# Performance work log

Hardware: AMD Instinct MI355X
Metric: run time of the kernel (lower is better)

Reference implementation:

```python
import jax, jax.numpy as jnp
import numpy as np

B, L, C = 128, 512, 8   # batch, stream length, path channels
DEPTH = 4
N_OUT = 10
SIG_DIM = C + C**2 + C**3 + C**4  # signatory.signature_channels(C, 4) = 4680


def setup_inputs() -> dict:
    key = jax.random.key(0)
    kx, kw, kb = jax.random.split(key, 3)
    X = jax.random.normal(kx, (B, L, C), dtype=jnp.float32) * 0.1
    W = jax.random.normal(kw, (N_OUT, SIG_DIM), dtype=jnp.float32) / np.sqrt(SIG_DIM)
    b = jax.random.normal(kb, (N_OUT,), dtype=jnp.float32) * 0.01
    return {"X": X, "W": W, "b": b}


def _signature_depth4(X):
    """Depth-4 path signature (Chen's relation scan), matching signatory.signature.

    X: (B, L, C) -> (B, C + C^2 + C^3 + C^4) with levels concatenated in order.
    """
    dx = X[:, 1:, :] - X[:, :-1, :]          # (B, L-1, C) path increments
    dx = jnp.swapaxes(dx, 0, 1)              # (L-1, B, C) for scan over stream
    bsz, c = X.shape[0], X.shape[2]

    def step(carry, v):
        s1, s2, s3, s4 = carry
        # exp(v) in the tensor algebra: e_k = v^{\otimes k} / k!
        e1 = v
        e2 = jnp.einsum('bi,bj->bij', v, v) / 2.0
        e3 = jnp.einsum('bij,bk->bijk', e2, v) / 3.0
        e4 = jnp.einsum('bijk,bl->bijkl', e3, v) / 4.0
        # Chen's relation: (S \otimes exp(v))_k = sum_i S_i \otimes e_{k-i}
        n1 = s1 + e1
        n2 = s2 + jnp.einsum('bi,bj->bij', s1, e1) + e2
        n3 = (s3 + jnp.einsum('bij,bk->bijk', s2, e1)
              + jnp.einsum('bi,bjk->bijk', s1, e2) + e3)
        n4 = (s4 + jnp.einsum('bijk,bl->bijkl', s3, e1)
              + jnp.einsum('bij,bkl->bijkl', s2, e2)
              + jnp.einsum('bi,bjkl->bijkl', s1, e3) + e4)
        return (n1, n2, n3, n4), None

    init = (jnp.zeros((bsz, c), X.dtype),
            jnp.zeros((bsz, c, c), X.dtype),
            jnp.zeros((bsz, c, c, c), X.dtype),
            jnp.zeros((bsz, c, c, c, c), X.dtype))
    (s1, s2, s3, s4), _ = jax.lax.scan(step, init, dx)
    return jnp.concatenate([s1.reshape(bsz, -1), s2.reshape(bsz, -1),
                            s3.reshape(bsz, -1), s4.reshape(bsz, -1)], axis=-1)


def reference(X, W, b):
    sig = _signature_depth4(X)               # (B, SIG_DIM)
    out = sig @ W.T + b                      # nn.Linear
    return out.reshape(-1, N_OUT)
```

## Files before the change

### kernel.cpp

```cpp
#include <hip/hip_runtime.h>

#define BATCH 128
#define LEN 512
#define N_OUT 10
#define SIG_DIM 4680
#define OFF2W 8
#define OFF3W 72
#define OFF4W 584
#define B2OFF 8
#define B3OFF 72
#define B4OFF 648
#define BUFSZ 4808

typedef float v4f __attribute__((ext_vector_type(4)));

__device__ __forceinline__ void stage_fat(float* __restrict__ buf,
                                          float s1, float s2,
                                          const float s3[8], const float s4[8][8],
                                          int lane) {
    if ((lane & 7) == 0) buf[lane >> 3] = s1;
    buf[B2OFF + lane] = s2;
    #pragma unroll
    for (int k = 0; k < 8; ++k) buf[B3OFF + lane * 9 + k] = s3[k];
    #pragma unroll
    for (int k = 0; k < 8; ++k) {
        #pragma unroll
        for (int l = 0; l < 8; ++l)
            buf[B4OFF + lane * 65 + k * 8 + l] = s4[k][l];
    }
}

__device__ __forceinline__ void combine_fat(float& A1, float& A2,
                                            float A3[8], float A4[8][8],
                                            const float* __restrict__ buf,
                                            int i, int j, int lane) {
    float B1[8];
    #pragma unroll
    for (int l = 0; l < 8; ++l) B1[l] = buf[l];
    #pragma unroll
    for (int k = 0; k < 8; ++k) {
        #pragma unroll
        for (int l = 0; l < 8; ++l) {
            A4[k][l] += A3[k] * B1[l]
                      + A2 * buf[B2OFF + k * 8 + l]
                      + A1 * buf[B3OFF + (j * 8 + k) * 9 + l]
                      + buf[B4OFF + lane * 65 + k * 8 + l];
        }
    }
    #pragma unroll
    for (int k = 0; k < 8; ++k) {
        A3[k] += A2 * B1[k]
               + A1 * buf[B2OFF + j * 8 + k]
               + buf[B3OFF + lane * 9 + k];
    }
    A2 += A1 * B1[j] + buf[B2OFF + lane];
    A1 += B1[i];
}

__global__ __launch_bounds__(512) void sig_fused_kernel(const float* __restrict__ X,
                                                        const float* __restrict__ W,
                                                        const float* __restrict__ bias,
                                                        float* __restrict__ out) {
    const int b = blockIdx.x;
    const int t = threadIdx.x;
    const int w = t >> 6;
    const int lane = t & 63;
    const int i = lane >> 3, j = lane & 7;

    __shared__ __align__(16) float lds[4 * BUFSZ];
    __shared__ float red[8][N_OUT];

    {
        const float2* __restrict__ X2 = (const float2*)(X + (size_t)b * LEN * 8);
        float2* __restrict__ d2 = (float2*)lds;
        #pragma unroll
        for (int p = 0; p < 4; ++p) {
            const int q = t + p * 512;
            const int s = q >> 2;
            float2 r = make_float2(0.f, 0.f);
            if (s < LEN - 1) {
                const float2 a = X2[q], c = X2[q + 4];
                r = make_float2(c.x - a.x, c.y - a.y);
            }
            d2[q] = r;
        }
    }
    __syncthreads();

    float s1 = 0.f, s2 = 0.f;
    float s3[8] = {};
    float s4[8][8] = {};
    {
        const int s0 = w * 64;
        const int nst = (w == 7) ? 63 : 64;
        const v4f* __restrict__ Xv = (const v4f*)(X + (size_t)b * LEN * 8);
        v4f pA = Xv[s0 * 2], pB = Xv[s0 * 2 + 1];
        const v4f* __restrict__ Xn = Xv + (s0 + 1) * 2;
        const float* __restrict__ dxL = lds + s0 * 8;
        #pragma unroll 4
        for (int s = 0; s < nst; ++s) {
            const v4f cA = Xn[s * 2], cB = Xn[s * 2 + 1];
            const v4f dA = cA - pA, dB = cB - pB;
            pA = cA; pB = cB;
            const float vi = dxL[s * 8 + i];
            const float vj = dxL[s * 8 + j];
            const float dv[8] = {dA.x, dA.y, dA.z, dA.w, dB.x, dB.y, dB.z, dB.w};

            const float t1 = s1 * vj;
            const float p  = vi * vj;
            const float u  = fmaf(1.f / 24.f, p, fmaf(1.f / 6.f, t1, 0.5f * s2));
            const float ww = fmaf(1.f / 6.f, p, fmaf(0.5f, t1, s2));
            float cc[8];
            #pragma unroll
            for (int k = 0; k < 8; ++k) {
                cc[k] = fmaf(dv[k], u, s3[k]);
                s3[k] = fmaf(dv[k], ww, s3[k]);
            }
            #pragma unroll
            for (int k = 0; k < 8; ++k) {
                #pragma unroll
                for (int l = 0; l < 8; ++l)
                    s4[k][l] = fmaf(cc[k], dv[l], s4[k][l]);
            }
            s2 = fmaf(0.5f, p, s2 + t1);
            s1 += vi;
        }
    }
    __syncthreads();

    float* __restrict__ buf0 = lds;
    float* __restrict__ buf1 = lds + BUFSZ;
    float* __restrict__ buf2 = lds + 2 * BUFSZ;
    float* __restrict__ buf3 = lds + 3 * BUFSZ;

    if (w == 1) stage_fat(buf0, s1, s2, s3, s4, lane);
    if (w == 3) stage_fat(buf1, s1, s2, s3, s4, lane);
    if (w == 5) stage_fat(buf2, s1, s2, s3, s4, lane);
    if (w == 7) stage_fat(buf3, s1, s2, s3, s4, lane);
    __syncthreads();
    if (w == 0) combine_fat(s1, s2, s3, s4, buf0, i, j, lane);
    if (w == 2) combine_fat(s1, s2, s3, s4, buf1, i, j, lane);
    if (w == 4) combine_fat(s1, s2, s3, s4, buf2, i, j, lane);
    if (w == 6) combine_fat(s1, s2, s3, s4, buf3, i, j, lane);
    __syncthreads();
    if (w == 2) stage_fat(buf0, s1, s2, s3, s4, lane);
    if (w == 6) stage_fat(buf1, s1, s2, s3, s4, lane);
    __syncthreads();
    if (w == 0) combine_fat(s1, s2, s3, s4, buf0, i, j, lane);
    if (w == 4) combine_fat(s1, s2, s3, s4, buf1, i, j, lane);
    __syncthreads();
    if (w == 4) stage_fat(buf0, s1, s2, s3, s4, lane);
    __syncthreads();
    if (w == 0) combine_fat(s1, s2, s3, s4, buf0, i, j, lane);
    __syncthreads();
    if (w == 0) stage_fat(buf0, s1, s2, s3, s4, lane);
    __syncthreads();

    const int ij = t >> 3, kk = t & 7;
    const float myA3 = buf0[B3OFF + ij * 9 + kk];
    float myA4[8];
    #pragma unroll
    for (int l = 0; l < 8; ++l) myA4[l] = buf0[B4OFF + ij * 65 + kk * 8 + l];
    const float myA2 = buf0[B2OFF + ij];
    const float myA1 = buf0[t >> 6];

    float part[N_OUT];
    #pragma unroll
    for (int n = 0; n < N_OUT; ++n) {
        const float* __restrict__ Wn = W + (size_t)n * SIG_DIM;
        float p = myA3 * Wn[OFF3W + t];
        const float4 w4a = *(const float4*)&Wn[OFF4W + t * 8];
        const float4 w4b = *(const float4*)&Wn[OFF4W + t * 8 + 4];
        p = fmaf(myA4[0], w4a.x, p);
        p = fmaf(myA4[1], w4a.y, p);
        p = fmaf(myA4[2], w4a.z, p);
        p = fmaf(myA4[3], w4a.w, p);
        p = fmaf(myA4[4], w4b.x, p);
        p = fmaf(myA4[5], w4b.y, p);
        p = fmaf(myA4[6], w4b.z, p);
        p = fmaf(myA4[7], w4b.w, p);
        if ((t & 7) == 0)  p = fmaf(myA2, Wn[OFF2W + (t >> 3)], p);
        if ((t & 63) == 0) p = fmaf(myA1, Wn[t >> 6], p);
        part[n] = p;
    }

    #pragma unroll
    for (int n = 0; n < N_OUT; ++n) {
        #pragma unroll
        for (int off = 32; off > 0; off >>= 1)
            part[n] += __shfl_xor(part[n], off, 64);
    }
    if (lane == 0) {
        #pragma unroll
        for (int n = 0; n < N_OUT; ++n) red[w][n] = part[n];
    }
    __syncthreads();
    if (t < N_OUT) {
        float s = bias[t];
        #pragma unroll
        for (int q = 0; q < 8; ++q) s += red[q][t];
        out[b * N_OUT + t] = s;
    }
}

extern "C" void kernel_launch(void* const* d_in, const int* in_sizes, int n_in,
                              void* d_out, int out_size, void* d_ws, size_t ws_size,
                              hipStream_t stream) {
    const float* X    = (const float*)d_in[0];
    const float* W    = (const float*)d_in[1];
    const float* bias = (const float*)d_in[2];
    float* out = (float*)d_out;
    (void)d_ws; (void)ws_size;

    hipLaunchKernelGGL(sig_fused_kernel, dim3(BATCH), dim3(512), 0, stream,
                       X, W, bias, out);
}
```

Baseline: 34.09 us.

## Split each path into four chunks across blocks and combine with Chen in second kernel

Each batch's 511 increments are now split over four blocks of 16 steps per wave instead of one block with 64 steps per wave. The per-chunk signatures go to workspace, and a second kernel merges them with Chen's relation and applies the linear layer. This shortens the serial scan per block and puts 512 blocks on the GPU instead of 128. In exchange it adds a second launch, a global round trip of the partial signatures, and extra combine work.

```diff
diff --git a/kernel.cpp b/kernel.cpp
--- a/kernel.cpp
+++ b/kernel.cpp
@@ -2,11 +2,12 @@
 
 #define BATCH 128
 #define LEN 512
+#define NCHUNK 4
+#define SIG_DIM 4680
 #define N_OUT 10
-#define SIG_DIM 4680
-#define OFF2W 8
-#define OFF3W 72
-#define OFF4W 584
+#define OFF2 8
+#define OFF3 72
+#define OFF4 584
 #define B2OFF 8
 #define B3OFF 72
 #define B4OFF 648
@@ -57,33 +58,27 @@
     A1 += B1[i];
 }
 
-__global__ __launch_bounds__(512) void sig_fused_kernel(const float* __restrict__ X,
-                                                        const float* __restrict__ W,
-                                                        const float* __restrict__ bias,
-                                                        float* __restrict__ out) {
-    const int b = blockIdx.x;
+__global__ __launch_bounds__(512) void sig_quarter_kernel(const float* __restrict__ X,
+                                                          float* __restrict__ sig) {
+    const int blk = blockIdx.x;
+    const int b = blk >> 2, q = blk & 3;
     const int t = threadIdx.x;
     const int w = t >> 6;
     const int lane = t & 63;
     const int i = lane >> 3, j = lane & 7;
+    const int s0base = q * 128;
 
     __shared__ __align__(16) float lds[4 * BUFSZ];
-    __shared__ float red[8][N_OUT];
 
     {
-        const float2* __restrict__ X2 = (const float2*)(X + (size_t)b * LEN * 8);
-        float2* __restrict__ d2 = (float2*)lds;
-        #pragma unroll
-        for (int p = 0; p < 4; ++p) {
-            const int q = t + p * 512;
-            const int s = q >> 2;
-            float2 r = make_float2(0.f, 0.f);
-            if (s < LEN - 1) {
-                const float2 a = X2[q], c = X2[q + 4];
-                r = make_float2(c.x - a.x, c.y - a.y);
-            }
-            d2[q] = r;
+        const float2* __restrict__ X2 =
+            (const float2*)(X + ((size_t)b * LEN + s0base) * 8);
+        float2 r = make_float2(0.f, 0.f);
+        if (s0base + (t >> 2) < LEN - 1) {
+            const float2 a = X2[t], c = X2[t + 4];
+            r = make_float2(c.x - a.x, c.y - a.y);
         }
+        ((float2*)lds)[t] = r;
     }
     __syncthreads();
 
@@ -91,12 +86,12 @@
     float s3[8] = {};
     float s4[8][8] = {};
     {
-        const int s0 = w * 64;
-        const int nst = (w == 7) ? 63 : 64;
+        const int s0 = s0base + w * 16;
+        const int nst = (s0 + 16 <= LEN - 1) ? 16 : (LEN - 1 - s0);
         const v4f* __restrict__ Xv = (const v4f*)(X + (size_t)b * LEN * 8);
         v4f pA = Xv[s0 * 2], pB = Xv[s0 * 2 + 1];
         const v4f* __restrict__ Xn = Xv + (s0 + 1) * 2;
-        const float* __restrict__ dxL = lds + s0 * 8;
+        const float* __restrict__ dxL = lds + (w * 16) * 8;
         #pragma unroll 4
         for (int s = 0; s < nst; ++s) {
             const v4f cA = Xn[s * 2], cB = Xn[s * 2 + 1];
@@ -156,31 +151,103 @@
     if (w == 0) stage_fat(buf0, s1, s2, s3, s4, lane);
     __syncthreads();
 
+    float* __restrict__ o = sig + (size_t)blk * SIG_DIM;
     const int ij = t >> 3, kk = t & 7;
-    const float myA3 = buf0[B3OFF + ij * 9 + kk];
-    float myA4[8];
-    #pragma unroll
-    for (int l = 0; l < 8; ++l) myA4[l] = buf0[B4OFF + ij * 65 + kk * 8 + l];
-    const float myA2 = buf0[B2OFF + ij];
-    const float myA1 = buf0[t >> 6];
+    if (t < 8)  o[t] = buf0[t];
+    if (t < 64) o[OFF2 + t] = buf0[B2OFF + t];
+    o[OFF3 + t] = buf0[B3OFF + ij * 9 + kk];
+    {
+        const float* __restrict__ src = &buf0[B4OFF + ij * 65 + kk * 8];
+        *(float4*)&o[OFF4 + t * 8] =
+            make_float4(src[0], src[1], src[2], src[3]);
+        *(float4*)&o[OFF4 + t * 8 + 4] =
+            make_float4(src[4], src[5], src[6], src[7]);
+    }
+}
+
+__device__ __forceinline__ void chen_combine(float& A1, float& A2, float& A3,
+                                             float A4[8],
+                                             const float* __restrict__ B,
+                                             int i, int j, int k, int t) {
+    const float B1i = B[i], B1j = B[j], B1k = B[k];
+    const float4 b1a = *(const float4*)&B[0];
+    const float4 b1b = *(const float4*)&B[4];
+    const float B2ij = B[OFF2 + i * 8 + j];
+    const float B2jk = B[OFF2 + j * 8 + k];
+    const float4 b2a = *(const float4*)&B[OFF2 + k * 8];
+    const float4 b2b = *(const float4*)&B[OFF2 + k * 8 + 4];
+    const float B3ijk = B[OFF3 + t];
+    const float4 b3a = *(const float4*)&B[OFF3 + (j * 8 + k) * 8];
+    const float4 b3b = *(const float4*)&B[OFF3 + (j * 8 + k) * 8 + 4];
+    const float4 b4a = *(const float4*)&B[OFF4 + t * 8];
+    const float4 b4b = *(const float4*)&B[OFF4 + t * 8 + 4];
+
+    A4[0] += A3 * b1a.x + A2 * b2a.x + A1 * b3a.x + b4a.x;
+    A4[1] += A3 * b1a.y + A2 * b2a.y + A1 * b3a.y + b4a.y;
+    A4[2] += A3 * b1a.z + A2 * b2a.z + A1 * b3a.z + b4a.z;
+    A4[3] += A3 * b1a.w + A2 * b2a.w + A1 * b3a.w + b4a.w;
+    A4[4] += A3 * b1b.x + A2 * b2b.x + A1 * b3b.x + b4b.x;
+    A4[5] += A3 * b1b.y + A2 * b2b.y + A1 * b3b.y + b4b.y;
+    A4[6] += A3 * b1b.z + A2 * b2b.z + A1 * b3b.z + b4b.z;
+    A4[7] += A3 * b1b.w + A2 * b2b.w + A1 * b3b.w + b4b.w;
+    A3 += A2 * B1k + A1 * B2jk + B3ijk;
+    A2 += A1 * B1j + B2ij;
+    A1 += B1i;
+}
+
+__global__ __launch_bounds__(512) void sig_combine_linear(const float* __restrict__ sig,
+                                                          const float* __restrict__ W,
+                                                          const float* __restrict__ bias,
+                                                          float* __restrict__ out) {
+    const int b = blockIdx.x;
+    const int t = threadIdx.x;
+    const int i = t >> 6, j = (t >> 3) & 7, k = t & 7;
+    const float* __restrict__ S = sig + (size_t)b * NCHUNK * SIG_DIM;
+
+    float A1 = S[i];
+    float A2 = S[OFF2 + i * 8 + j];
+    float A3 = S[OFF3 + t];
+    const float4 a4a = *(const float4*)&S[OFF4 + t * 8];
+    const float4 a4b = *(const float4*)&S[OFF4 + t * 8 + 4];
+    float A4[8] = {a4a.x, a4a.y, a4a.z, a4a.w, a4b.x, a4b.y, a4b.z, a4b.w};
+    chen_combine(A1, A2, A3, A4, S + SIG_DIM, i, j, k, t);
+
+    const float* __restrict__ S2 = S + 2 * SIG_DIM;
+    float C1 = S2[i];
+    float C2 = S2[OFF2 + i * 8 + j];
+    float C3 = S2[OFF3 + t];
+    const float4 c4a = *(const float4*)&S2[OFF4 + t * 8];
+    const float4 c4b = *(const float4*)&S2[OFF4 + t * 8 + 4];
+    float C4[8] = {c4a.x, c4a.y, c4a.z, c4a.w, c4b.x, c4b.y, c4b.z, c4b.w};
+    chen_combine(C1, C2, C3, C4, S2 + SIG_DIM, i, j, k, t);
+
+    __shared__ __align__(16) float Bs[SIG_DIM];
+    if ((t & 63) == 0) Bs[t >> 6] = C1;
+    if ((t & 7) == 0)  Bs[OFF2 + (t >> 3)] = C2;
+    Bs[OFF3 + t] = C3;
+    *(float4*)&Bs[OFF4 + t * 8]     = make_float4(C4[0], C4[1], C4[2], C4[3]);
+    *(float4*)&Bs[OFF4 + t * 8 + 4] = make_float4(C4[4], C4[5], C4[6], C4[7]);
+    __syncthreads();
+
+    chen_combine(A1, A2, A3, A4, Bs, i, j, k, t);
 
     float part[N_OUT];
     #pragma unroll
     for (int n = 0; n < N_OUT; ++n) {
         const float* __restrict__ Wn = W + (size_t)n * SIG_DIM;
-        float p = myA3 * Wn[OFF3W + t];
-        const float4 w4a = *(const float4*)&Wn[OFF4W + t * 8];
-        const float4 w4b = *(const float4*)&Wn[OFF4W + t * 8 + 4];
-        p = fmaf(myA4[0], w4a.x, p);
-        p = fmaf(myA4[1], w4a.y, p);
-        p = fmaf(myA4[2], w4a.z, p);
-        p = fmaf(myA4[3], w4a.w, p);
-        p = fmaf(myA4[4], w4b.x, p);
-        p = fmaf(myA4[5], w4b.y, p);
-        p = fmaf(myA4[6], w4b.z, p);
-        p = fmaf(myA4[7], w4b.w, p);
-        if ((t & 7) == 0)  p = fmaf(myA2, Wn[OFF2W + (t >> 3)], p);
-        if ((t & 63) == 0) p = fmaf(myA1, Wn[t >> 6], p);
+        float p = A3 * Wn[OFF3 + t];
+        const float4 w4a = *(const float4*)&Wn[OFF4 + t * 8];
+        const float4 w4b = *(const float4*)&Wn[OFF4 + t * 8 + 4];
+        p = fmaf(A4[0], w4a.x, p);
+        p = fmaf(A4[1], w4a.y, p);
+        p = fmaf(A4[2], w4a.z, p);
+        p = fmaf(A4[3], w4a.w, p);
+        p = fmaf(A4[4], w4b.x, p);
+        p = fmaf(A4[5], w4b.y, p);
+        p = fmaf(A4[6], w4b.z, p);
+        p = fmaf(A4[7], w4b.w, p);
+        if ((t & 7) == 0)  p = fmaf(A2, Wn[OFF2 + (t >> 3)], p);
+        if ((t & 63) == 0) p = fmaf(A1, Wn[t >> 6], p);
         part[n] = p;
     }
 
@@ -190,15 +257,17 @@
         for (int off = 32; off > 0; off >>= 1)
             part[n] += __shfl_xor(part[n], off, 64);
     }
-    if (lane == 0) {
-        #pragma unroll
-        for (int n = 0; n < N_OUT; ++n) red[w][n] = part[n];
+    __shared__ float red[8][N_OUT];
+    const int wv = t >> 6, ln = t & 63;
+    if (ln == 0) {
+        #pragma unroll
+        for (int n = 0; n < N_OUT; ++n) red[wv][n] = part[n];
     }
     __syncthreads();
     if (t < N_OUT) {
         float s = bias[t];
         #pragma unroll
-        for (int q = 0; q < 8; ++q) s += red[q][t];
+        for (int w = 0; w < 8; ++w) s += red[w][t];
         out[b * N_OUT + t] = s;
     }
 }
@@ -210,8 +279,8 @@
     const float* W    = (const float*)d_in[1];
     const float* bias = (const float*)d_in[2];
     float* out = (float*)d_out;
-    (void)d_ws; (void)ws_size;
-
-    hipLaunchKernelGGL(sig_fused_kernel, dim3(BATCH), dim3(512), 0, stream,
-                       X, W, bias, out);
-}
+    float* sig = (float*)d_ws;
+
+    hipLaunchKernelGGL(sig_quarter_kernel, dim3(BATCH * NCHUNK), dim3(512), 0, stream, X, sig);
+    hipLaunchKernelGGL(sig_combine_linear, dim3(BATCH), dim3(512), 0, stream, sig, W, bias, out);
+}
```

Result: slower. 43.28 us (+27.0%).
